# Kernel optimization log

Hardware: AMD Instinct MI355X
Metric: run time of the kernel (lower is better)

The kernel has to match this reference:

```python
import jax, jax.numpy as jnp
import numpy as np

B, C, H, W = 4, 128, 64, 64


def setup_inputs() -> dict:
    key = jax.random.key(0)
    ks = jax.random.split(key, 7)
    s = 1.0 / np.sqrt(C)
    return {
        "x": jax.random.normal(ks[0], (B, C, H, W), dtype=jnp.float32),
        "Wq": jax.random.normal(ks[1], (C, C), dtype=jnp.float32) * s,
        "bq": jnp.zeros((C,), dtype=jnp.float32),
        "Wk": jax.random.normal(ks[2], (C, C), dtype=jnp.float32) * s,
        "bk": jnp.zeros((C,), dtype=jnp.float32),
        "Wv": jax.random.normal(ks[3], (C, C), dtype=jnp.float32) * s,
        "bv": jnp.zeros((C,), dtype=jnp.float32),
    }


def reference(x, Wq, bq, Wk, bk, Wv, bv):
    b, c, h, w = x.shape
    n = h * w
    scale = c ** (-0.5)
    # tokens: [B, N, C]
    xt = x.reshape(b, c, n).transpose(0, 2, 1)
    # 1x1 convs == per-token channel GEMMs (out[c'] = sum_c W[c',c] x[c] + b[c'])
    q = jnp.einsum("bnc,dc->bnd", xt, Wq) + bq  # [B, N, C]
    k = jnp.einsum("bnc,dc->bnd", xt, Wk) + bk  # [B, N, C]
    v = jnp.einsum("bnc,dc->bnd", xt, Wv) + bv  # [B, N, C]
    scores = jnp.einsum("bic,bjc->bij", q, k) * scale  # [B, N, N]
    attn = jax.nn.softmax(scores, axis=-1)
    out = jnp.einsum("bij,bjc->bic", attn, v)  # [B, N, C]
    return out.transpose(0, 2, 1).reshape(b, c, h, w)
```

## Files before the change

### kernel.cpp

```cpp
#include <hip/hip_runtime.h>
#include <hip/hip_bf16.h>


#define BATCH 4
#define CH    128
#define NTOK  4096
#define TK    64
#define SCALE 0.08838834764831845f
#define LOG2E 1.4426950408889634f
#define MFIX  16.0f
#define PSTR  72

typedef __attribute__((ext_vector_type(8)))  short short8;
typedef __attribute__((ext_vector_type(4)))  float f32x4;
typedef __attribute__((ext_vector_type(16))) float f32x16;

static __device__ __forceinline__ unsigned short f2bf(float f) {
    __hip_bfloat16 h = (__hip_bfloat16)f;
    return *(const unsigned short*)&h;
}

__global__ __launch_bounds__(256) void convert_w_kernel(
    const float* __restrict__ Wq, const float* __restrict__ Wk,
    const float* __restrict__ Wv, unsigned short* __restrict__ wb)
{
    const int idx = (blockIdx.x * 256 + threadIdx.x) * 4;
    const float* srcs[3] = {Wq, Wk, Wv};
    #pragma unroll
    for (int m = 0; m < 3; ++m) {
        float4 v = *(const float4*)(srcs[m] + idx);
        unsigned short o[4] = {f2bf(v.x), f2bf(v.y), f2bf(v.z), f2bf(v.w)};
        *(uint2*)(wb + (size_t)m * CH * CH + idx) = *(const uint2*)o;
    }
}

__global__ __launch_bounds__(256) void proj_mfma_kernel(
    const float* __restrict__ x,
    const unsigned short* __restrict__ wqb, const unsigned short* __restrict__ wkb,
    const unsigned short* __restrict__ wvb,
    const float* __restrict__ bq, const float* __restrict__ bk,
    const float* __restrict__ bv,
    unsigned short* __restrict__ q_ws, unsigned short* __restrict__ k_ws,
    unsigned short* __restrict__ vt_ws)
{
    __shared__ __align__(16) unsigned short XsT[64 * CH];

    const int t    = threadIdx.x;
    const int w    = t >> 6;
    const int lane = t & 63;
    const int quad = lane >> 4;
    const int c16  = lane & 15;
    const int n0   = blockIdx.x * 64;
    const int b    = blockIdx.y;
    const float* xb = x + (size_t)b * CH * NTOK;

    {
        const int tok = lane;
        #pragma unroll
        for (int cc = 0; cc < 4; ++cc) {
            const int cb = 32 * w + 8 * cc;
            unsigned short tmp[8];
            #pragma unroll
            for (int j = 0; j < 8; ++j)
                tmp[j] = f2bf(xb[(size_t)(cb + j) * NTOK + n0 + tok]);
            const int phys = ((cb >> 3) ^ (tok & 15));
            *(short8*)&XsT[tok * CH + phys * 8] = *(const short8*)tmp;
        }
    }
    __syncthreads();

    short8 xa[4];
    #pragma unroll
    for (int ks = 0; ks < 4; ++ks)
        xa[ks] = *(const short8*)&XsT[(16 * w + c16) * CH + (((4 * ks + quad) ^ c16) << 3)];

    #pragma unroll
    for (int nt = 0; nt < 8; ++nt) {
        f32x4 aq = (f32x4){0.f, 0.f, 0.f, 0.f};
        f32x4 ak = (f32x4){0.f, 0.f, 0.f, 0.f};
        const unsigned short* wqr = wqb + (16 * nt + c16) * CH;
        const unsigned short* wkr = wkb + (16 * nt + c16) * CH;
        #pragma unroll
        for (int ks = 0; ks < 4; ++ks) {
            const short8 bqf = *(const short8*)(wqr + 32 * ks + 8 * quad);
            const short8 bkf = *(const short8*)(wkr + 32 * ks + 8 * quad);
            aq = __builtin_amdgcn_mfma_f32_16x16x32_bf16(xa[ks], bqf, aq, 0, 0, 0);
            ak = __builtin_amdgcn_mfma_f32_16x16x32_bf16(xa[ks], bkf, ak, 0, 0, 0);
        }
        const float bqv = bq[16 * nt + c16];
        const float bkv = bk[16 * nt + c16];
        #pragma unroll
        for (int r = 0; r < 4; ++r) {
            const int n = n0 + 16 * w + quad * 4 + r;
            const size_t o = ((size_t)b * NTOK + n) * CH + 16 * nt + c16;
            q_ws[o] = f2bf((aq[r] + bqv) * (SCALE * LOG2E));
            k_ws[o] = f2bf(ak[r] + bkv);
        }
    }

    short8 wva[2][4];
    float  bvv[2][4];
    #pragma unroll
    for (int mt = 0; mt < 2; ++mt) {
        const int crow16 = 16 * (2 * w + mt);
        #pragma unroll
        for (int ks = 0; ks < 4; ++ks)
            wva[mt][ks] = *(const short8*)&wvb[(crow16 + c16) * CH + 32 * ks + 8 * quad];
        #pragma unroll
        for (int r = 0; r < 4; ++r)
            bvv[mt][r] = bv[crow16 + quad * 4 + r];
    }
    #pragma unroll
    for (int nt = 0; nt < 4; ++nt) {
        short8 xbf[4];
        #pragma unroll
        for (int ks = 0; ks < 4; ++ks)
            xbf[ks] = *(const short8*)&XsT[(16 * nt + c16) * CH + (((4 * ks + quad) ^ c16) << 3)];
        #pragma unroll
        for (int mt = 0; mt < 2; ++mt) {
            f32x4 acc = (f32x4){0.f, 0.f, 0.f, 0.f};
            #pragma unroll
            for (int ks = 0; ks < 4; ++ks)
                acc = __builtin_amdgcn_mfma_f32_16x16x32_bf16(wva[mt][ks], xbf[ks], acc, 0, 0, 0);
            #pragma unroll
            for (int r = 0; r < 4; ++r) {
                const int crow = 16 * (2 * w + mt) + quad * 4 + r;
                vt_ws[((size_t)b * CH + crow) * NTOK + n0 + 16 * nt + c16] =
                    f2bf(acc[r] + bvv[mt][r]);
            }
        }
    }
}

template <int SPLIT>
__global__ __launch_bounds__(256, 2) void flash_attn_mfma(
    const unsigned short* __restrict__ q_ws,
    const unsigned short* __restrict__ k_ws,
    const unsigned short* __restrict__ vt_ws,
    float* __restrict__ out,
    float* __restrict__ Op, float* __restrict__ l_p)
{
    __shared__ __align__(16) unsigned short KsU[TK * CH];
    __shared__ __align__(16) unsigned short VtU[CH * TK];
    __shared__ __align__(16) unsigned short PlU[4 * 32 * PSTR];

    const int t    = threadIdx.x;
    const int w    = t >> 6;
    const int lane = t & 63;
    const int half = lane >> 5;
    const int l32  = lane & 31;
    const int jc   = blockIdx.y;
    const int b    = blockIdx.z;
    const int n0   = blockIdx.x * 128;
    const int jbeg = jc * (NTOK / SPLIT);
    const int jend = jbeg + (NTOK / SPLIT);

    short8 qa[8];
    {
        const unsigned short* qrow = q_ws + ((size_t)b * NTOK + n0 + 32 * w + l32) * CH;
        #pragma unroll
        for (int ks = 0; ks < 8; ++ks)
            qa[ks] = *(const short8*)(qrow + ks * 16 + half * 8);
    }

    f32x16 Oa[4];
    #pragma unroll
    for (int ct = 0; ct < 4; ++ct) Oa[ct] = (f32x16)(0.0f);
    f32x16 La = (f32x16)(0.0f);

    const unsigned short* kg = k_ws  + (size_t)b * NTOK * CH;
    const unsigned short* vg = vt_ws + (size_t)b * CH * NTOK;
    const short8 ones8 = (short8)(short)0x3F80;
    unsigned short* Pw = &PlU[w * 32 * PSTR];

    for (int j0 = jbeg; j0 < jend; j0 += TK) {
        __syncthreads();

        {
            const int rl = lane >> 4, u = lane & 15;
            #pragma unroll
            for (int ci = 0; ci < 4; ++ci) {
                const int row = 16 * w + 4 * ci + rl;
                const int g   = u ^ (row & 15);
                const unsigned short* src = kg + (size_t)(j0 + row) * CH + g * 8;
                __builtin_amdgcn_global_load_lds(
                    (const __attribute__((address_space(1))) void*)src,
                    (__attribute__((address_space(3))) void*)&KsU[(16 * w + 4 * ci) * CH],
                    16, 0, 0);
            }
        }
        {
            const int cl = lane >> 3, u = lane & 7;
            #pragma unroll
            for (int ci = 0; ci < 4; ++ci) {
                const int c = 32 * w + 8 * ci + cl;
                const int g = u ^ (c & 7);
                const unsigned short* src = vg + (size_t)c * NTOK + j0 + g * 8;
                __builtin_amdgcn_global_load_lds(
                    (const __attribute__((address_space(1))) void*)src,
                    (__attribute__((address_space(3))) void*)&VtU[(32 * w + 8 * ci) * TK],
                    16, 0, 0);
            }
        }
        __syncthreads();

        f32x16 s0 = (f32x16)(-MFIX);
        f32x16 s1 = (f32x16)(-MFIX);
        #pragma unroll
        for (int ks = 0; ks < 8; ++ks) {
            const int ph = (2 * ks + half) ^ (l32 & 15);
            const short8 kf0 = *(const short8*)&KsU[l32 * CH + ph * 8];
            const short8 kf1 = *(const short8*)&KsU[(32 + l32) * CH + ph * 8];
            s0 = __builtin_amdgcn_mfma_f32_32x32x16_bf16(qa[ks], kf0, s0, 0, 0, 0);
            s1 = __builtin_amdgcn_mfma_f32_32x32x16_bf16(qa[ks], kf1, s1, 0, 0, 0);
        }

        #pragma unroll
        for (int reg = 0; reg < 16; ++reg) {
            const int row = (reg & 3) + 8 * (reg >> 2) + 4 * half;
            Pw[row * PSTR + l32]      = f2bf(exp2f(s0[reg]));
            Pw[row * PSTR + 32 + l32] = f2bf(exp2f(s1[reg]));
        }
        __threadfence_block();

        #pragma unroll
        for (int ks2 = 0; ks2 < 4; ++ks2) {
            const short8 pa = *(const short8*)&Pw[l32 * PSTR + ks2 * 16 + half * 8];
            #pragma unroll
            for (int ct = 0; ct < 4; ++ct) {
                const int ch = ct * 32 + l32;
                const int ph = (2 * ks2 + half) ^ (ch & 7);
                const short8 vf = *(const short8*)&VtU[ch * TK + ph * 8];
                Oa[ct] = __builtin_amdgcn_mfma_f32_32x32x16_bf16(pa, vf, Oa[ct], 0, 0, 0);
            }
            La = __builtin_amdgcn_mfma_f32_32x32x16_bf16(pa, ones8, La, 0, 0, 0);
        }
    }

    if constexpr (SPLIT == 1) {
        #pragma unroll
        for (int reg = 0; reg < 16; ++reg) {
            const int row = (reg & 3) + 8 * (reg >> 2) + 4 * half;
            const int n = n0 + 32 * w + row;
            const float inv = 1.0f / La[reg];
            #pragma unroll
            for (int ct = 0; ct < 4; ++ct)
                out[((size_t)b * CH + ct * 32 + l32) * NTOK + n] = Oa[ct][reg] * inv;
        }
    } else {
        const size_t chunk = (size_t)(b * SPLIT + jc);
        #pragma unroll
        for (int reg = 0; reg < 16; ++reg) {
            const int row = (reg & 3) + 8 * (reg >> 2) + 4 * half;
            const int n = n0 + 32 * w + row;
            const size_t base = (chunk * NTOK + n) * CH;
            #pragma unroll
            for (int ct = 0; ct < 4; ++ct)
                Op[base + ct * 32 + l32] = Oa[ct][reg];
            if (l32 == 0) l_p[chunk * NTOK + n] = La[reg];
        }
    }
}

template <int SPLIT>
__global__ __launch_bounds__(256) void combine_kernel(
    const float* __restrict__ Op, const float* __restrict__ l_p,
    float* __restrict__ out)
{
    const int t  = threadIdx.x;
    const int cg = t & 31;
    const int r8 = t >> 5;
    const int n0 = blockIdx.x * 64;
    const int b  = blockIdx.y;

    for (int it = 0; it < 8; ++it) {
        const int n = n0 + it * 8 + r8;
        float den = 0.f;
        float4 acc = make_float4(0.f, 0.f, 0.f, 0.f);
        #pragma unroll
        for (int j = 0; j < SPLIT; ++j) {
            const size_t chunk = (size_t)(b * SPLIT + j);
            den += l_p[chunk * NTOK + n];
            const float4 o = *(const float4*)&Op[(chunk * NTOK + n) * CH + cg * 4];
            acc.x += o.x; acc.y += o.y; acc.z += o.z; acc.w += o.w;
        }
        const float inv = 1.0f / den;
        out[((size_t)b * CH + cg * 4 + 0) * NTOK + n] = acc.x * inv;
        out[((size_t)b * CH + cg * 4 + 1) * NTOK + n] = acc.y * inv;
        out[((size_t)b * CH + cg * 4 + 2) * NTOK + n] = acc.z * inv;
        out[((size_t)b * CH + cg * 4 + 3) * NTOK + n] = acc.w * inv;
    }
}

extern "C" void kernel_launch(void* const* d_in, const int* in_sizes, int n_in,
                              void* d_out, int out_size, void* d_ws, size_t ws_size,
                              hipStream_t stream) {
    const float* x  = (const float*)d_in[0];
    const float* Wq = (const float*)d_in[1];
    const float* bq = (const float*)d_in[2];
    const float* Wk = (const float*)d_in[3];
    const float* bk = (const float*)d_in[4];
    const float* Wv = (const float*)d_in[5];
    const float* bv = (const float*)d_in[6];
    float* out = (float*)d_out;

    const size_t QKV = (size_t)BATCH * NTOK * CH;
    unsigned short* q_ws  = (unsigned short*)d_ws;
    unsigned short* k_ws  = q_ws + QKV;
    unsigned short* vt_ws = k_ws + QKV;
    unsigned short* wb    = vt_ws + QKV;
    float* Op = (float*)(wb + 3 * CH * CH);

    const size_t baseBytes = 3 * QKV * 2 + 3 * CH * CH * 2;
    auto needBytes = [&](size_t S) {
        return baseBytes + S * BATCH * NTOK * (size_t)(CH * 4 + 4);
    };

    convert_w_kernel<<<CH * CH / (256 * 4), 256, 0, stream>>>(Wq, Wk, Wv, wb);

    dim3 gp(NTOK / 64, BATCH);
    proj_mfma_kernel<<<gp, 256, 0, stream>>>(x, wb, wb + CH * CH, wb + 2 * CH * CH,
                                             bq, bk, bv, q_ws, k_ws, vt_ws);

    if (ws_size >= needBytes(8)) {
        float* l_p = Op + (size_t)8 * BATCH * NTOK * CH;
        dim3 ga(NTOK / 128, 8, BATCH);
        flash_attn_mfma<8><<<ga, 256, 0, stream>>>(q_ws, k_ws, vt_ws, out, Op, l_p);
        dim3 gc(NTOK / 64, BATCH);
        combine_kernel<8><<<gc, 256, 0, stream>>>(Op, l_p, out);
    } else if (ws_size >= needBytes(4)) {
        float* l_p = Op + (size_t)4 * BATCH * NTOK * CH;
        dim3 ga(NTOK / 128, 4, BATCH);
        flash_attn_mfma<4><<<ga, 256, 0, stream>>>(q_ws, k_ws, vt_ws, out, Op, l_p);
        dim3 gc(NTOK / 64, BATCH);
        combine_kernel<4><<<gc, 256, 0, stream>>>(Op, l_p, out);
    } else {
        dim3 ga(NTOK / 128, 1, BATCH);
        flash_attn_mfma<1><<<ga, 256, 0, stream>>>(q_ws, k_ws, vt_ws, out,
                                                   nullptr, nullptr);
    }
}
```

Before: 146.2 us.

## Replace MFMA projection and weight conversion with fp32 VALU per-output projection kernel

Drops the separate weight bf16 conversion kernel and the LDS-staged MFMA projection, replacing them with a simple kernel where each thread computes one output channel for one token in fp32 using FMAs. This removes one launch and the bf16 rounding of weights and x. The cost is that each block rereads the x column for all 128 output channels and does the work on vector ALUs instead of matrix cores. The combine kernel also switches to 32 tokens per block, which doubles its grid size.

```diff
diff --git a/kernel.cpp b/kernel.cpp
--- a/kernel.cpp
+++ b/kernel.cpp
@@ -12,7 +12,6 @@
 #define PSTR  72
 
 typedef __attribute__((ext_vector_type(8)))  short short8;
-typedef __attribute__((ext_vector_type(4)))  float f32x4;
 typedef __attribute__((ext_vector_type(16))) float f32x16;
 
 static __device__ __forceinline__ unsigned short f2bf(float f) {
@@ -20,116 +19,34 @@
     return *(const unsigned short*)&h;
 }
 
-__global__ __launch_bounds__(256) void convert_w_kernel(
-    const float* __restrict__ Wq, const float* __restrict__ Wk,
-    const float* __restrict__ Wv, unsigned short* __restrict__ wb)
-{
-    const int idx = (blockIdx.x * 256 + threadIdx.x) * 4;
-    const float* srcs[3] = {Wq, Wk, Wv};
-    #pragma unroll
-    for (int m = 0; m < 3; ++m) {
-        float4 v = *(const float4*)(srcs[m] + idx);
-        unsigned short o[4] = {f2bf(v.x), f2bf(v.y), f2bf(v.z), f2bf(v.w)};
-        *(uint2*)(wb + (size_t)m * CH * CH + idx) = *(const uint2*)o;
-    }
-}
-
-__global__ __launch_bounds__(256) void proj_mfma_kernel(
+__global__ __launch_bounds__(256) void proj_valu_kernel(
     const float* __restrict__ x,
-    const unsigned short* __restrict__ wqb, const unsigned short* __restrict__ wkb,
-    const unsigned short* __restrict__ wvb,
-    const float* __restrict__ bq, const float* __restrict__ bk,
-    const float* __restrict__ bv,
-    unsigned short* __restrict__ q_ws, unsigned short* __restrict__ k_ws,
+    const float* __restrict__ Wq, const float* __restrict__ bq,
+    const float* __restrict__ Wk, const float* __restrict__ bk,
+    const float* __restrict__ Wv, const float* __restrict__ bv,
+    unsigned short* __restrict__ q_ws,
+    unsigned short* __restrict__ k_ws,
     unsigned short* __restrict__ vt_ws)
 {
-    __shared__ __align__(16) unsigned short XsT[64 * CH];
-
-    const int t    = threadIdx.x;
-    const int w    = t >> 6;
-    const int lane = t & 63;
-    const int quad = lane >> 4;
-    const int c16  = lane & 15;
-    const int n0   = blockIdx.x * 64;
-    const int b    = blockIdx.y;
+    const int n = blockIdx.x * blockDim.x + threadIdx.x;
+    const int d = blockIdx.y;
+    const int b = blockIdx.z;
     const float* xb = x + (size_t)b * CH * NTOK;
 
-    {
-        const int tok = lane;
-        #pragma unroll
-        for (int cc = 0; cc < 4; ++cc) {
-            const int cb = 32 * w + 8 * cc;
-            unsigned short tmp[8];
-            #pragma unroll
-            for (int j = 0; j < 8; ++j)
-                tmp[j] = f2bf(xb[(size_t)(cb + j) * NTOK + n0 + tok]);
-            const int phys = ((cb >> 3) ^ (tok & 15));
-            *(short8*)&XsT[tok * CH + phys * 8] = *(const short8*)tmp;
-        }
-    }
-    __syncthreads();
-
-    short8 xa[4];
-    #pragma unroll
-    for (int ks = 0; ks < 4; ++ks)
-        xa[ks] = *(const short8*)&XsT[(16 * w + c16) * CH + (((4 * ks + quad) ^ c16) << 3)];
-
-    #pragma unroll
-    for (int nt = 0; nt < 8; ++nt) {
-        f32x4 aq = (f32x4){0.f, 0.f, 0.f, 0.f};
-        f32x4 ak = (f32x4){0.f, 0.f, 0.f, 0.f};
-        const unsigned short* wqr = wqb + (16 * nt + c16) * CH;
-        const unsigned short* wkr = wkb + (16 * nt + c16) * CH;
-        #pragma unroll
-        for (int ks = 0; ks < 4; ++ks) {
-            const short8 bqf = *(const short8*)(wqr + 32 * ks + 8 * quad);
-            const short8 bkf = *(const short8*)(wkr + 32 * ks + 8 * quad);
-            aq = __builtin_amdgcn_mfma_f32_16x16x32_bf16(xa[ks], bqf, aq, 0, 0, 0);
-            ak = __builtin_amdgcn_mfma_f32_16x16x32_bf16(xa[ks], bkf, ak, 0, 0, 0);
-        }
-        const float bqv = bq[16 * nt + c16];
-        const float bkv = bk[16 * nt + c16];
-        #pragma unroll
-        for (int r = 0; r < 4; ++r) {
-            const int n = n0 + 16 * w + quad * 4 + r;
-            const size_t o = ((size_t)b * NTOK + n) * CH + 16 * nt + c16;
-            q_ws[o] = f2bf((aq[r] + bqv) * (SCALE * LOG2E));
-            k_ws[o] = f2bf(ak[r] + bkv);
-        }
-    }
-
-    short8 wva[2][4];
-    float  bvv[2][4];
-    #pragma unroll
-    for (int mt = 0; mt < 2; ++mt) {
-        const int crow16 = 16 * (2 * w + mt);
-        #pragma unroll
-        for (int ks = 0; ks < 4; ++ks)
-            wva[mt][ks] = *(const short8*)&wvb[(crow16 + c16) * CH + 32 * ks + 8 * quad];
-        #pragma unroll
-        for (int r = 0; r < 4; ++r)
-            bvv[mt][r] = bv[crow16 + quad * 4 + r];
-    }
-    #pragma unroll
-    for (int nt = 0; nt < 4; ++nt) {
-        short8 xbf[4];
-        #pragma unroll
-        for (int ks = 0; ks < 4; ++ks)
-            xbf[ks] = *(const short8*)&XsT[(16 * nt + c16) * CH + (((4 * ks + quad) ^ c16) << 3)];
-        #pragma unroll
-        for (int mt = 0; mt < 2; ++mt) {
-            f32x4 acc = (f32x4){0.f, 0.f, 0.f, 0.f};
-            #pragma unroll
-            for (int ks = 0; ks < 4; ++ks)
-                acc = __builtin_amdgcn_mfma_f32_16x16x32_bf16(wva[mt][ks], xbf[ks], acc, 0, 0, 0);
-            #pragma unroll
-            for (int r = 0; r < 4; ++r) {
-                const int crow = 16 * (2 * w + mt) + quad * 4 + r;
-                vt_ws[((size_t)b * CH + crow) * NTOK + n0 + 16 * nt + c16] =
-                    f2bf(acc[r] + bvv[mt][r]);
-            }
-        }
-    }
+    float aq = bq[d];
+    float ak = bk[d];
+    float av = bv[d];
+    #pragma unroll 8
+    for (int c = 0; c < CH; ++c) {
+        const float xv = xb[(size_t)c * NTOK + n];
+        aq = fmaf(Wq[d * CH + c], xv, aq);
+        ak = fmaf(Wk[d * CH + c], xv, ak);
+        av = fmaf(Wv[d * CH + c], xv, av);
+    }
+    const size_t o = ((size_t)b * NTOK + n) * CH + d;
+    q_ws[o] = f2bf(aq * (SCALE * LOG2E));
+    k_ws[o] = f2bf(ak);
+    vt_ws[((size_t)b * CH + d) * NTOK + n] = f2bf(av);
 }
 
 template <int SPLIT>
@@ -270,10 +187,10 @@
     const int t  = threadIdx.x;
     const int cg = t & 31;
     const int r8 = t >> 5;
-    const int n0 = blockIdx.x * 64;
+    const int n0 = blockIdx.x * 32;
     const int b  = blockIdx.y;
 
-    for (int it = 0; it < 8; ++it) {
+    for (int it = 0; it < 4; ++it) {
         const int n = n0 + it * 8 + r8;
         float den = 0.f;
         float4 acc = make_float4(0.f, 0.f, 0.f, 0.f);
@@ -308,31 +225,28 @@
     unsigned short* q_ws  = (unsigned short*)d_ws;
     unsigned short* k_ws  = q_ws + QKV;
     unsigned short* vt_ws = k_ws + QKV;
-    unsigned short* wb    = vt_ws + QKV;
-    float* Op = (float*)(wb + 3 * CH * CH);
-
-    const size_t baseBytes = 3 * QKV * 2 + 3 * CH * CH * 2;
+    float* Op = (float*)(vt_ws + QKV);
+
+    const size_t baseBytes = 3 * QKV * 2;
     auto needBytes = [&](size_t S) {
         return baseBytes + S * BATCH * NTOK * (size_t)(CH * 4 + 4);
     };
 
-    convert_w_kernel<<<CH * CH / (256 * 4), 256, 0, stream>>>(Wq, Wk, Wv, wb);
-
-    dim3 gp(NTOK / 64, BATCH);
-    proj_mfma_kernel<<<gp, 256, 0, stream>>>(x, wb, wb + CH * CH, wb + 2 * CH * CH,
-                                             bq, bk, bv, q_ws, k_ws, vt_ws);
+    dim3 gp(NTOK / 256, CH, BATCH);
+    proj_valu_kernel<<<gp, 256, 0, stream>>>(x, Wq, bq, Wk, bk, Wv, bv,
+                                             q_ws, k_ws, vt_ws);
 
     if (ws_size >= needBytes(8)) {
         float* l_p = Op + (size_t)8 * BATCH * NTOK * CH;
         dim3 ga(NTOK / 128, 8, BATCH);
         flash_attn_mfma<8><<<ga, 256, 0, stream>>>(q_ws, k_ws, vt_ws, out, Op, l_p);
-        dim3 gc(NTOK / 64, BATCH);
+        dim3 gc(NTOK / 32, BATCH);
         combine_kernel<8><<<gc, 256, 0, stream>>>(Op, l_p, out);
     } else if (ws_size >= needBytes(4)) {
         float* l_p = Op + (size_t)4 * BATCH * NTOK * CH;
         dim3 ga(NTOK / 128, 4, BATCH);
         flash_attn_mfma<4><<<ga, 256, 0, stream>>>(q_ws, k_ws, vt_ws, out, Op, l_p);
-        dim3 gc(NTOK / 64, BATCH);
+        dim3 gc(NTOK / 32, BATCH);
         combine_kernel<4><<<gc, 256, 0, stream>>>(Op, l_p, out);
     } else {
         dim3 ga(NTOK / 128, 1, BATCH);
```

Measured after the change: 179.8 us. +22.9%, slower.
